# Kernel optimization log

Measured on AMD Instinct MI355X. Metric: run time of the kernel, lower is better.

The kernel has to match this reference:

```python
import jax, jax.numpy as jnp
import numpy as np

B, T, I, H, NC = 128, 512, 128, 512, 100


def setup_inputs() -> dict:
    key = jax.random.key(0)
    ks = jax.random.split(key, 16)
    x = jax.random.randint(ks[0], (B, T, 1), 0, NC + 1)
    # embedding table with padding row 0 zeroed (padding_idx=0)
    emb = (jax.random.normal(ks[1], (NC + 1, I)) * 1.0).at[0].set(0.0)
    # kaiming_normal_ fan_out, sigmoid nonlinearity -> std = 1/sqrt(fan_out)
    sx = 1.0 / np.sqrt(H)
    sc = 1.0 / np.sqrt(H)
    sp = 1.0 / np.sqrt(NC)
    return {
        "x": x,
        "emb": emb,
        "Wfx": jax.random.normal(ks[2], (I, H)) * sx,
        "Wfc": jax.random.normal(ks[3], (H, H)) * sc,
        "bf": jnp.zeros((H,)),
        "Wix": jax.random.normal(ks[4], (I, H)) * sx,
        "Wic": jax.random.normal(ks[5], (H, H)) * sc,
        "bi": jnp.zeros((H,)),
        "Wox": jax.random.normal(ks[6], (I, H)) * sx,
        "Woc": jax.random.normal(ks[7], (H, H)) * sc,
        "bo": jnp.zeros((H,)),
        "Wcx": jax.random.normal(ks[8], (I, H)) * sx,
        "bc": jnp.zeros((H,)),
        "Wph": jax.random.normal(ks[9], (H, NC)) * sp,
        "bp": jnp.zeros((NC,)),
    }


def reference(x, emb, Wfx, Wfc, bf, Wix, Wic, bi, Wox, Woc, bo, Wcx, bc, Wph, bp):
    idx = x[:, :, 0]                      # [B,T] int indices
    xe = emb[idx]                         # [B,T,I] embedded inputs
    h_dim = Wfc.shape[0]
    # Fuse the four input-side GEMMs into one, hoisted out of the recurrence.
    Wx = jnp.concatenate([Wfx, Wix, Wox, Wcx], axis=1)   # [I,4H]
    bx = jnp.concatenate([bf, bi, bo, bc])               # [4H]
    xg = jnp.einsum('bti,ih->bth', xe, Wx) + bx          # [B,T,4H]
    # Fuse the three peephole (cell-state) GEMMs into one per step.
    Wc = jnp.concatenate([Wfc, Wic, Woc], axis=1)        # [H,3H]
    reset = (idx > 0).astype(xg.dtype)                   # [B,T]

    def step(carry, inp):
        C, h = carry
        g, r = inp                        # g: [B,4H], r: [B]
        cg = C @ Wc                       # [B,3H]
        f = jax.nn.sigmoid(g[:, :h_dim] + cg[:, :h_dim])
        i = jax.nn.sigmoid(g[:, h_dim:2 * h_dim] + cg[:, h_dim:2 * h_dim])
        o = jax.nn.sigmoid(g[:, 2 * h_dim:3 * h_dim] + cg[:, 2 * h_dim:])
        c_tilde = jax.nn.sigmoid(g[:, 3 * h_dim:])        # note: sigmoid, not tanh (per source)
        Cn = (c_tilde * i + C * f) * r[:, None]           # reset on padding tokens
        hn = jnp.tanh(Cn) * o
        return (Cn, hn), None

    bsz = xg.shape[0]
    init = (jnp.zeros((bsz, h_dim), xg.dtype), jnp.zeros((bsz, h_dim), xg.dtype))
    xs = (jnp.swapaxes(xg, 0, 1), jnp.swapaxes(reset, 0, 1))  # time-major
    (Cf, hf), _ = jax.lax.scan(step, init, xs)
    p = hf @ Wph + bp                     # [B,num_classes]
    return jax.nn.log_softmax(p, axis=1)
```

## Files before the change

### kernel.cpp

```cpp
#include <hip/hip_runtime.h>
#include <hip/hip_bf16.h>
#include <stdint.h>

#define HD   512
#define ID   128
#define NCLS 100
#define TT   512
#define BB   128
#define NEMB 101
#define NGRP 32
#define GWG  8
#define RPG  4
#define COLS 64
#define THR  512
#define CPAD 640
#define CBW  260
#define PST  5

#define WS_FLAG 0
#define WS_BAR  4096
#define WS_G    65536
#define WS_C0   (1u * 1024 * 1024)
#define WS_C1   (WS_C0 + 262144)
#define WS_HFB  (WS_C1 + 262144)
#define NBARU   4096

using bf16 = __hip_bfloat16;

__device__ __forceinline__ float b2f(bf16 v) { return __bfloat162float(v); }
__device__ __forceinline__ float sigf(float x) { return 1.0f / (1.0f + expf(-x)); }

__device__ __forceinline__ float cld(const float* p) {
    return __hip_atomic_load(p, __ATOMIC_RELAXED, __HIP_MEMORY_SCOPE_AGENT);
}
__device__ __forceinline__ void cst(float* p, float v) {
    __hip_atomic_store(p, v, __ATOMIC_RELAXED, __HIP_MEMORY_SCOPE_AGENT);
}
__device__ __forceinline__ uint64_t cld8(const float* p) {
    return __hip_atomic_load((const uint64_t*)p, __ATOMIC_RELAXED,
                             __HIP_MEMORY_SCOPE_AGENT);
}

__device__ __forceinline__ uint32_t pkbf(float x, float y) {
    uint32_t u;
    asm("v_cvt_pk_bf16_f32 %0, %1, %2" : "=v"(u) : "v"(x), "v"(y));
    return u;
}
#define DOT2(acc, w, c) \
    asm("v_dot2_f32_bf16 %0, %1, %2, %0" : "+v"(acc) : "v"(w), "v"(c))

template <bool BF>
__device__ __forceinline__ float ldv(const void* p, int i) {
    if constexpr (BF) return b2f(((const bf16*)p)[i]);
    else              return ((const float*)p)[i];
}

__device__ __forceinline__ int cpi(int h) { return (h >> 4) * 20 + (h & 15); }

__device__ __forceinline__ void gbarrier(unsigned* cnt, unsigned* iter) {
    __syncthreads();
    if (threadIdx.x == 0) {
        __hip_atomic_fetch_add(cnt, 1u, __ATOMIC_RELAXED, __HIP_MEMORY_SCOPE_AGENT);
        const unsigned tgt = (*iter + 1u) * GWG;
        while (__hip_atomic_load(cnt, __ATOMIC_RELAXED, __HIP_MEMORY_SCOPE_AGENT) < tgt)
            ;
    }
    ++*iter;
    __syncthreads();
}

__global__ void init_k(const uint32_t* __restrict__ emb_raw,
                       int* __restrict__ flag, unsigned* __restrict__ bars) {
    const int t = threadIdx.x;
    for (int k = t; k < NBARU; k += 1024) bars[k] = 0u;
    if (t == 0) {
        uint32_t acc = 0;
        for (int i = 64; i < 128; ++i) acc |= emb_raw[i];
        *flag = (acc == 0u) ? 0 : 1;
    }
}

template <bool BF>
__global__ void build_G(const int* __restrict__ flag,
                        const void* __restrict__ emb,
                        const void* __restrict__ Wfx, const void* __restrict__ Wix,
                        const void* __restrict__ Wox, const void* __restrict__ Wcx,
                        const void* __restrict__ bfv, const void* __restrict__ biv,
                        const void* __restrict__ bov, const void* __restrict__ bcv,
                        float* __restrict__ G) {
    if (*flag != (BF ? 1 : 0)) return;
    const int c   = blockIdx.x;
    const int j   = blockIdx.y * 256 + threadIdx.x;
    const int q   = j >> 9;
    const int col = j & 511;
    const void* W  = (q == 0) ? Wfx : (q == 1) ? Wix : (q == 2) ? Wox : Wcx;
    const void* bv = (q == 0) ? bfv : (q == 1) ? biv : (q == 2) ? bov : bcv;
    float acc = ldv<BF>(bv, col);
    for (int i = 0; i < ID; ++i)
        acc += ldv<BF>(emb, c * ID + i) * ldv<BF>(W, i * HD + col);
    if (q == 3) acc = sigf(acc);
    G[c * 2048 + j] = acc;
}

template <bool BF>
__global__ __launch_bounds__(THR, 2) void recur_bs(
    const int* __restrict__ flag, const int* __restrict__ x,
    const float* __restrict__ G,
    const void* __restrict__ Wfc, const void* __restrict__ Wic,
    const void* __restrict__ Woc,
    float* __restrict__ C0, float* __restrict__ C1,
    float* __restrict__ Hfb, unsigned* __restrict__ bars)
{
    if (*flag != (BF ? 1 : 0)) return;

    __shared__ __align__(16) float Cs[RPG * CPAD];
    __shared__ __align__(8)  float2 part2[2048 * PST];
    __shared__ int idx[RPG * TT];
    __shared__ int lz[RPG];

    const int blk   = blockIdx.x;
    const int grp   = blk >> 3;
    const int rank  = blk & 7;
    const int r0    = grp * RPG;
    const int h0    = rank * COLS;
    const int tid   = threadIdx.x;
    const int cp    = tid & 15;
    const int chunk = tid >> 4;
    unsigned* bar = bars + grp * 32;

    idx[tid]        = x[r0 * TT + tid];
    idx[tid + 512]  = x[r0 * TT + tid + 512];
    idx[tid + 1024] = x[r0 * TT + tid + 1024];
    idx[tid + 1536] = x[r0 * TT + tid + 1536];
    if (tid < RPG) lz[tid] = -1;
    __syncthreads();
    #pragma unroll
    for (int r = 0; r < RPG; ++r)
        if (idx[r * TT + tid] == 0) atomicMax(&lz[r], tid);
    __syncthreads();
    int t0 = TT;
    #pragma unroll
    for (int r = 0; r < RPG; ++r) t0 = min(t0, lz[r] + 1);

    unsigned bi = 0;
    float Creg = 0.0f;
    const bool isUpd = (tid < COLS * RPG);
    const int uc = tid & 63, ur = tid >> 6;
    const int pe = cpi(tid);

    if constexpr (BF) {
        const uint16_t* Wfr = (const uint16_t*)Wfc;
        const uint16_t* Wir = (const uint16_t*)Wic;

        uint32_t wf0[8], wf1[8], wf2[8], wf3[8];
        uint32_t wi0[8], wi1[8], wi2[8], wi3[8];
        #pragma unroll
        for (int p = 0; p < 8; ++p) {
            const int hp = chunk * 16 + 2 * p;
            const int b0 = hp * HD + h0 + cp, b1 = (hp + 1) * HD + h0 + cp;
            wf0[p] = (uint32_t)Wfr[b0]      | ((uint32_t)Wfr[b1]      << 16);
            wf1[p] = (uint32_t)Wfr[b0 + 16] | ((uint32_t)Wfr[b1 + 16] << 16);
            wf2[p] = (uint32_t)Wfr[b0 + 32] | ((uint32_t)Wfr[b1 + 32] << 16);
            wf3[p] = (uint32_t)Wfr[b0 + 48] | ((uint32_t)Wfr[b1 + 48] << 16);
            wi0[p] = (uint32_t)Wir[b0]      | ((uint32_t)Wir[b1]      << 16);
            wi1[p] = (uint32_t)Wir[b0 + 16] | ((uint32_t)Wir[b1 + 16] << 16);
            wi2[p] = (uint32_t)Wir[b0 + 32] | ((uint32_t)Wir[b1 + 32] << 16);
            wi3[p] = (uint32_t)Wir[b0 + 48] | ((uint32_t)Wir[b1 + 48] << 16);
        }
        #pragma unroll
        for (int p = 0; p < 8; ++p)
            asm volatile("" : "+v"(wf0[p]), "+v"(wf1[p]), "+v"(wf2[p]), "+v"(wf3[p]),
                              "+v"(wi0[p]), "+v"(wi1[p]), "+v"(wi2[p]), "+v"(wi3[p]));

        if (isUpd) {
            cst(&C0[(r0 + ur) * HD + h0 + uc], 0.0f);
            cst(&C1[(r0 + ur) * HD + h0 + uc], 0.0f);
        }
        gbarrier(bar, &bi);

        uint32_t* Cb = (uint32_t*)Cs;
        const int srow = tid >> 8;
        const int spr  = tid & 255;

        for (int t = t0; t < TT; ++t) {
            #pragma unroll
            for (int p = 0; p < 8; ++p)
                asm volatile("" : "+v"(wf0[p]), "+v"(wf1[p]), "+v"(wf2[p]), "+v"(wf3[p]),
                                  "+v"(wi0[p]), "+v"(wi1[p]), "+v"(wi2[p]), "+v"(wi3[p]));

            const float* cur = (t & 1) ? C1 : C0;
            float*       nxt = (t & 1) ? C0 : C1;

            float gf = 0.f, gi = 0.f, sgc = 0.f;
            int cl = 1;
            if (isUpd) {
                cl = idx[ur * TT + t];
                const float* Gr = G + cl * 2048;
                gf  = Gr[h0 + uc];
                gi  = Gr[512 + h0 + uc];
                sgc = Gr[1536 + h0 + uc];
            }

            {
                const uint64_t a = cld8(cur + (r0 + srow) * HD + 2 * spr);
                const uint64_t b = cld8(cur + (r0 + srow + 2) * HD + 2 * spr);
                const uint32_t pa = pkbf(__uint_as_float((uint32_t)a),
                                         __uint_as_float((uint32_t)(a >> 32)));
                const uint32_t pb = pkbf(__uint_as_float((uint32_t)b),
                                         __uint_as_float((uint32_t)(b >> 32)));
                Cb[srow * CBW + spr]       = pa;
                Cb[(srow + 2) * CBW + spr] = pb;
            }
            __syncthreads();

            float f0[RPG], f1[RPG], f2[RPG], f3[RPG];
            float i0[RPG], i1[RPG], i2[RPG], i3[RPG];
            #pragma unroll
            for (int r = 0; r < RPG; ++r) {
                f0[r] = 0.f; f1[r] = 0.f; f2[r] = 0.f; f3[r] = 0.f;
                i0[r] = 0.f; i1[r] = 0.f; i2[r] = 0.f; i3[r] = 0.f;
            }
            {
                const int cb = chunk * 8;
                #pragma unroll
                for (int hh = 0; hh < 2; ++hh) {
                    #pragma unroll
                    for (int r = 0; r < RPG; ++r) {
                        const uint4 cv = *reinterpret_cast<const uint4*>(
                            Cb + r * CBW + cb + 4 * hh);
                        const int p = 4 * hh;
                        DOT2(f0[r], wf0[p + 0], cv.x); DOT2(f0[r], wf0[p + 1], cv.y);
                        DOT2(f0[r], wf0[p + 2], cv.z); DOT2(f0[r], wf0[p + 3], cv.w);
                        DOT2(f1[r], wf1[p + 0], cv.x); DOT2(f1[r], wf1[p + 1], cv.y);
                        DOT2(f1[r], wf1[p + 2], cv.z); DOT2(f1[r], wf1[p + 3], cv.w);
                        DOT2(f2[r], wf2[p + 0], cv.x); DOT2(f2[r], wf2[p + 1], cv.y);
                        DOT2(f2[r], wf2[p + 2], cv.z); DOT2(f2[r], wf2[p + 3], cv.w);
                        DOT2(f3[r], wf3[p + 0], cv.x); DOT2(f3[r], wf3[p + 1], cv.y);
                        DOT2(f3[r], wf3[p + 2], cv.z); DOT2(f3[r], wf3[p + 3], cv.w);
                        DOT2(i0[r], wi0[p + 0], cv.x); DOT2(i0[r], wi0[p + 1], cv.y);
                        DOT2(i0[r], wi0[p + 2], cv.z); DOT2(i0[r], wi0[p + 3], cv.w);
                        DOT2(i1[r], wi1[p + 0], cv.x); DOT2(i1[r], wi1[p + 1], cv.y);
                        DOT2(i1[r], wi1[p + 2], cv.z); DOT2(i1[r], wi1[p + 3], cv.w);
                        DOT2(i2[r], wi2[p + 0], cv.x); DOT2(i2[r], wi2[p + 1], cv.y);
                        DOT2(i2[r], wi2[p + 2], cv.z); DOT2(i2[r], wi2[p + 3], cv.w);
                        DOT2(i3[r], wi3[p + 0], cv.x); DOT2(i3[r], wi3[p + 1], cv.y);
                        DOT2(i3[r], wi3[p + 2], cv.z); DOT2(i3[r], wi3[p + 3], cv.w);
                    }
                }
            }
            {
                float2* p0 = part2 + (chunk * 64 + cp)      * PST;
                float2* p1 = part2 + (chunk * 64 + cp + 16) * PST;
                float2* p2 = part2 + (chunk * 64 + cp + 32) * PST;
                float2* p3 = part2 + (chunk * 64 + cp + 48) * PST;
                #pragma unroll
                for (int r = 0; r < RPG; ++r) {
                    p0[r] = make_float2(f0[r], i0[r]);
                    p1[r] = make_float2(f1[r], i1[r]);
                    p2[r] = make_float2(f2[r], i2[r]);
                    p3[r] = make_float2(f3[r], i3[r]);
                }
            }
            __syncthreads();

            if (isUpd) {
                float df = 0.f, di = 0.f;
                #pragma unroll
                for (int ch = 0; ch < 32; ++ch) {
                    const float2 v = part2[(ch * 64 + uc) * PST + ur];
                    df += v.x;
                    di += v.y;
                }
                float Cn = sgc * sigf(gi + di) + Creg * sigf(gf + df);
                Cn = (cl > 0) ? Cn : 0.0f;
                Creg = Cn;
                cst(&nxt[(r0 + ur) * HD + h0 + uc], Cn);
            }
            gbarrier(bar, &bi);
        }
    } else {
        float wf0[16], wf1[16], wf2[16], wf3[16];
        float wi0[16], wi1[16], wi2[16], wi3[16];
        #pragma unroll
        for (int k = 0; k < 16; ++k) {
            const int hp = chunk * 16 + k;
            wf0[k] = ldv<BF>(Wfc, hp * HD + h0 + cp);
            wf1[k] = ldv<BF>(Wfc, hp * HD + h0 + cp + 16);
            wf2[k] = ldv<BF>(Wfc, hp * HD + h0 + cp + 32);
            wf3[k] = ldv<BF>(Wfc, hp * HD + h0 + cp + 48);
            wi0[k] = ldv<BF>(Wic, hp * HD + h0 + cp);
            wi1[k] = ldv<BF>(Wic, hp * HD + h0 + cp + 16);
            wi2[k] = ldv<BF>(Wic, hp * HD + h0 + cp + 32);
            wi3[k] = ldv<BF>(Wic, hp * HD + h0 + cp + 48);
        }
        #pragma unroll
        for (int k = 0; k < 16; ++k)
            asm volatile("" : "+v"(wf0[k]), "+v"(wf1[k]), "+v"(wf2[k]), "+v"(wf3[k]),
                              "+v"(wi0[k]), "+v"(wi1[k]), "+v"(wi2[k]), "+v"(wi3[k]));

        if (isUpd) {
            cst(&C0[(r0 + ur) * HD + h0 + uc], 0.0f);
            cst(&C1[(r0 + ur) * HD + h0 + uc], 0.0f);
        }
        gbarrier(bar, &bi);

        for (int t = t0; t < TT; ++t) {
            #pragma unroll
            for (int k = 0; k < 16; ++k)
                asm volatile("" : "+v"(wf0[k]), "+v"(wf1[k]), "+v"(wf2[k]), "+v"(wf3[k]),
                                  "+v"(wi0[k]), "+v"(wi1[k]), "+v"(wi2[k]), "+v"(wi3[k]));

            const float* cur = (t & 1) ? C1 : C0;
            float*       nxt = (t & 1) ? C0 : C1;

            float gf = 0.f, gi = 0.f, sgc = 0.f;
            int cl = 1;
            if (isUpd) {
                cl = idx[ur * TT + t];
                const float* Gr = G + cl * 2048;
                gf  = Gr[h0 + uc];
                gi  = Gr[512 + h0 + uc];
                sgc = Gr[1536 + h0 + uc];
            }

            {
                const float v0 = cld(cur + (r0 + 0) * HD + tid);
                const float v1 = cld(cur + (r0 + 1) * HD + tid);
                const float v2 = cld(cur + (r0 + 2) * HD + tid);
                const float v3 = cld(cur + (r0 + 3) * HD + tid);
                Cs[0 * CPAD + pe] = v0;
                Cs[1 * CPAD + pe] = v1;
                Cs[2 * CPAD + pe] = v2;
                Cs[3 * CPAD + pe] = v3;
            }
            __syncthreads();

            float f0[RPG], f1[RPG], f2[RPG], f3[RPG];
            float i0[RPG], i1[RPG], i2[RPG], i3[RPG];
            #pragma unroll
            for (int r = 0; r < RPG; ++r) {
                f0[r] = 0.f; f1[r] = 0.f; f2[r] = 0.f; f3[r] = 0.f;
                i0[r] = 0.f; i1[r] = 0.f; i2[r] = 0.f; i3[r] = 0.f;
            }
            {
                const int cb = chunk * 5;
                #pragma unroll
                for (int j = 0; j < 4; ++j) {
                    #pragma unroll
                    for (int r = 0; r < RPG; ++r) {
                        const float4 cv = reinterpret_cast<const float4*>(
                            Cs + r * CPAD)[cb + j];
                        f0[r] += wf0[4*j]*cv.x + wf0[4*j+1]*cv.y + wf0[4*j+2]*cv.z + wf0[4*j+3]*cv.w;
                        f1[r] += wf1[4*j]*cv.x + wf1[4*j+1]*cv.y + wf1[4*j+2]*cv.z + wf1[4*j+3]*cv.w;
                        f2[r] += wf2[4*j]*cv.x + wf2[4*j+1]*cv.y + wf2[4*j+2]*cv.z + wf2[4*j+3]*cv.w;
                        f3[r] += wf3[4*j]*cv.x + wf3[4*j+1]*cv.y + wf3[4*j+2]*cv.z + wf3[4*j+3]*cv.w;
                        i0[r] += wi0[4*j]*cv.x + wi0[4*j+1]*cv.y + wi0[4*j+2]*cv.z + wi0[4*j+3]*cv.w;
                        i1[r] += wi1[4*j]*cv.x + wi1[4*j+1]*cv.y + wi1[4*j+2]*cv.z + wi1[4*j+3]*cv.w;
                        i2[r] += wi2[4*j]*cv.x + wi2[4*j+1]*cv.y + wi2[4*j+2]*cv.z + wi2[4*j+3]*cv.w;
                        i3[r] += wi3[4*j]*cv.x + wi3[4*j+1]*cv.y + wi3[4*j+2]*cv.z + wi3[4*j+3]*cv.w;
                    }
                }
            }
            {
                float2* p0 = part2 + (chunk * 64 + cp)      * PST;
                float2* p1 = part2 + (chunk * 64 + cp + 16) * PST;
                float2* p2 = part2 + (chunk * 64 + cp + 32) * PST;
                float2* p3 = part2 + (chunk * 64 + cp + 48) * PST;
                #pragma unroll
                for (int r = 0; r < RPG; ++r) {
                    p0[r] = make_float2(f0[r], i0[r]);
                    p1[r] = make_float2(f1[r], i1[r]);
                    p2[r] = make_float2(f2[r], i2[r]);
                    p3[r] = make_float2(f3[r], i3[r]);
                }
            }
            __syncthreads();

            if (isUpd) {
                float df = 0.f, di = 0.f;
                #pragma unroll
                for (int ch = 0; ch < 32; ++ch) {
                    const float2 v = part2[(ch * 64 + uc) * PST + ur];
                    df += v.x;
                    di += v.y;
                }
                float Cn = sgc * sigf(gi + di) + Creg * sigf(gf + df);
                Cn = (cl > 0) ? Cn : 0.0f;
                Creg = Cn;
                cst(&nxt[(r0 + ur) * HD + h0 + uc], Cn);
            }
            gbarrier(bar, &bi);
        }
    }

    {
        const float v0 = cld(C1 + (r0 + 0) * HD + tid);
        const float v1 = cld(C1 + (r0 + 1) * HD + tid);
        const float v2 = cld(C1 + (r0 + 2) * HD + tid);
        const float v3 = cld(C1 + (r0 + 3) * HD + tid);
        Cs[0 * CPAD + pe] = v0;
        Cs[1 * CPAD + pe] = v1;
        Cs[2 * CPAD + pe] = v2;
        Cs[3 * CPAD + pe] = v3;
        __syncthreads();

        const int oc = tid & 63, och = tid >> 6;
        float ao[RPG];
        #pragma unroll
        for (int r = 0; r < RPG; ++r) ao[r] = 0.0f;
        #pragma unroll 4
        for (int k = 0; k < 64; ++k) {
            const int hp = och * 64 + k;
            const int hpp = cpi(hp);
            const float wo = ldv<BF>(Woc, hp * HD + h0 + oc);
            #pragma unroll
            for (int r = 0; r < RPG; ++r)
                ao[r] += wo * Cs[r * CPAD + hpp];
        }
        {
            float2* pp = part2 + (och * 64 + oc) * PST;
            #pragma unroll
            for (int r2 = 0; r2 < RPG / 2; ++r2)
                pp[r2] = make_float2(ao[2 * r2], ao[2 * r2 + 1]);
        }
        __syncthreads();
        if (isUpd) {
            float s = 0.f;
            #pragma unroll
            for (int ch = 0; ch < 8; ++ch) {
                const float2 v = part2[(ch * 64 + uc) * PST + (ur >> 1)];
                s += (ur & 1) ? v.y : v.x;
            }
            const int cl2 = idx[ur * TT + TT - 1];
            const float o = sigf(G[cl2 * 2048 + 1024 + h0 + uc] + s);
            Hfb[(r0 + ur) * HD + h0 + uc] = tanhf(Creg) * o;
        }
    }
}

template <bool BF>
__global__ __launch_bounds__(128) void proj(
    const int* __restrict__ flag, const float* __restrict__ Hfb,
    const void* __restrict__ Wph, const void* __restrict__ bp,
    void* __restrict__ out)
{
    if (*flag != (BF ? 1 : 0)) return;
    __shared__ __align__(16) float hv[HD];
    __shared__ float p_s[NCLS];
    __shared__ float lse_s;
    const int b   = blockIdx.x;
    const int tid = threadIdx.x;

    reinterpret_cast<float4*>(hv)[tid] =
        reinterpret_cast<const float4*>(Hfb + b * HD)[tid];
    __syncthreads();

    if (tid < NCLS) {
        float p = ldv<BF>(bp, tid);
        for (int h = 0; h < HD; ++h)
            p += hv[h] * ldv<BF>(Wph, h * NCLS + tid);
        p_s[tid] = p;
    }
    __syncthreads();
    if (tid == 0) {
        float m = -1e30f;
        for (int n = 0; n < NCLS; ++n) m = fmaxf(m, p_s[n]);
        float sum = 0.0f;
        for (int n = 0; n < NCLS; ++n) sum += expf(p_s[n] - m);
        lse_s = m + logf(sum);
    }
    __syncthreads();
    if (tid < NCLS) {
        const float v = p_s[tid] - lse_s;
        if constexpr (BF) ((bf16*)out)[b * NCLS + tid] = __float2bfloat16(v);
        else              ((float*)out)[b * NCLS + tid] = v;
    }
}

extern "C" void kernel_launch(void* const* d_in, const int* in_sizes, int n_in,
                              void* d_out, int out_size, void* d_ws, size_t ws_size,
                              hipStream_t stream) {
    const int*  x   = (const int*)d_in[0];
    const void* emb = d_in[1];
    const void* Wfx = d_in[2];
    const void* Wfc = d_in[3];
    const void* bfv = d_in[4];
    const void* Wix = d_in[5];
    const void* Wic = d_in[6];
    const void* biv = d_in[7];
    const void* Wox = d_in[8];
    const void* Woc = d_in[9];
    const void* bov = d_in[10];
    const void* Wcx = d_in[11];
    const void* bcv = d_in[12];
    const void* Wph = d_in[13];
    const void* bp  = d_in[14];

    int*      flag = (int*)((char*)d_ws + WS_FLAG);
    unsigned* bars = (unsigned*)((char*)d_ws + WS_BAR);
    float*    G    = (float*)((char*)d_ws + WS_G);
    float*    C0   = (float*)((char*)d_ws + WS_C0);
    float*    C1   = (float*)((char*)d_ws + WS_C1);
    float*    Hfb  = (float*)((char*)d_ws + WS_HFB);

    init_k<<<1, 1024, 0, stream>>>((const uint32_t*)emb, flag, bars);

    build_G<false><<<dim3(NEMB, 8), 256, 0, stream>>>(flag, emb, Wfx, Wix, Wox, Wcx,
                                                      bfv, biv, bov, bcv, G);
    build_G<true ><<<dim3(NEMB, 8), 256, 0, stream>>>(flag, emb, Wfx, Wix, Wox, Wcx,
                                                      bfv, biv, bov, bcv, G);

    {
        void* args[] = {(void*)&flag, (void*)&x, (void*)&G,
                        (void*)&Wfc, (void*)&Wic, (void*)&Woc,
                        (void*)&C0, (void*)&C1, (void*)&Hfb, (void*)&bars};
        hipLaunchCooperativeKernel((const void*)recur_bs<false>, dim3(NGRP * GWG), dim3(THR),
                                   args, 0, stream);
        hipLaunchCooperativeKernel((const void*)recur_bs<true>, dim3(NGRP * GWG), dim3(THR),
                                   args, 0, stream);
    }

    proj<false><<<BB, 128, 0, stream>>>(flag, Hfb, Wph, bp, d_out);
    proj<true ><<<BB, 128, 0, stream>>>(flag, Hfb, Wph, bp, d_out);
}
```

Baseline: 1.604 ms.

## Repartition bf16 recurrence into 64 groups of 4 workgroups with 2 rows each

The bf16 recurrence path now splits the batch into 64 groups of 2 rows, each handled by 4 workgroups covering 128 columns, instead of 32 groups of 4 rows spread over 8 workgroups. Fewer workgroups share each per-step global barrier, which is meant to cut barrier latency and cross-workgroup traffic on the serial time loop. In exchange each thread holds twice as many packed weight registers and does a longer dot product over fewer rows. This raises register pressure, and occupancy or spills could suffer. The fp32 path keeps the old partition, with constants renamed.

```diff
diff --git a/kernel.cpp b/kernel.cpp
--- a/kernel.cpp
+++ b/kernel.cpp
@@ -8,14 +8,21 @@
 #define TT   512
 #define BB   128
 #define NEMB 101
-#define NGRP 32
-#define GWG  8
-#define RPG  4
-#define COLS 64
 #define THR  512
+
+#define NGRPB 64
+#define GWGB  4
+#define RPGB  2
+#define COLSB 128
+#define NGRPF 32
+#define GWGF  8
+#define RPGF  4
+#define COLSF 64
+
 #define CPAD 640
 #define CBW  260
-#define PST  5
+#define PSTF 5
+#define PSTB 3
 
 #define WS_FLAG 0
 #define WS_BAR  4096
@@ -57,11 +64,11 @@
 
 __device__ __forceinline__ int cpi(int h) { return (h >> 4) * 20 + (h & 15); }
 
-__device__ __forceinline__ void gbarrier(unsigned* cnt, unsigned* iter) {
+__device__ __forceinline__ void gbarrier(unsigned* cnt, unsigned* iter, int gwg) {
     __syncthreads();
     if (threadIdx.x == 0) {
         __hip_atomic_fetch_add(cnt, 1u, __ATOMIC_RELAXED, __HIP_MEMORY_SCOPE_AGENT);
-        const unsigned tgt = (*iter + 1u) * GWG;
+        const unsigned tgt = (*iter + 1u) * (unsigned)gwg;
         while (__hip_atomic_load(cnt, __ATOMIC_RELAXED, __HIP_MEMORY_SCOPE_AGENT) < tgt)
             ;
     }
@@ -113,78 +120,75 @@
 {
     if (*flag != (BF ? 1 : 0)) return;
 
-    __shared__ __align__(16) float Cs[RPG * CPAD];
-    __shared__ __align__(8)  float2 part2[2048 * PST];
-    __shared__ int idx[RPG * TT];
-    __shared__ int lz[RPG];
-
-    const int blk   = blockIdx.x;
-    const int grp   = blk >> 3;
-    const int rank  = blk & 7;
-    const int r0    = grp * RPG;
-    const int h0    = rank * COLS;
-    const int tid   = threadIdx.x;
-    const int cp    = tid & 15;
-    const int chunk = tid >> 4;
-    unsigned* bar = bars + grp * 32;
-
-    idx[tid]        = x[r0 * TT + tid];
-    idx[tid + 512]  = x[r0 * TT + tid + 512];
-    idx[tid + 1024] = x[r0 * TT + tid + 1024];
-    idx[tid + 1536] = x[r0 * TT + tid + 1536];
-    if (tid < RPG) lz[tid] = -1;
-    __syncthreads();
-    #pragma unroll
-    for (int r = 0; r < RPG; ++r)
-        if (idx[r * TT + tid] == 0) atomicMax(&lz[r], tid);
-    __syncthreads();
-    int t0 = TT;
-    #pragma unroll
-    for (int r = 0; r < RPG; ++r) t0 = min(t0, lz[r] + 1);
-
+    __shared__ __align__(16) float Cs[RPGF * CPAD];
+    __shared__ __align__(8)  float2 part2[2048 * PSTF];
+    __shared__ int idx[RPGF * TT];
+    __shared__ int lz[RPGF];
+
+    const int blk = blockIdx.x;
+    const int tid = threadIdx.x;
     unsigned bi = 0;
-    float Creg = 0.0f;
-    const bool isUpd = (tid < COLS * RPG);
-    const int uc = tid & 63, ur = tid >> 6;
-    const int pe = cpi(tid);
 
     if constexpr (BF) {
+        const int grp   = blk >> 2;
+        const int rank  = blk & 3;
+        const int r0    = grp * RPGB;
+        const int h0    = rank * COLSB;
+        const int cp    = tid & 31;
+        const int chunk = tid >> 5;
+        unsigned* bar = bars + grp * 32;
+
+        idx[tid]       = x[r0 * TT + tid];
+        idx[tid + 512] = x[r0 * TT + tid + 512];
+        if (tid < RPGB) lz[tid] = -1;
+        __syncthreads();
+        #pragma unroll
+        for (int r = 0; r < RPGB; ++r)
+            if (idx[r * TT + tid] == 0) atomicMax(&lz[r], tid);
+        __syncthreads();
+        int t0 = TT;
+        #pragma unroll
+        for (int r = 0; r < RPGB; ++r) t0 = min(t0, lz[r] + 1);
+
         const uint16_t* Wfr = (const uint16_t*)Wfc;
         const uint16_t* Wir = (const uint16_t*)Wic;
-
-        uint32_t wf0[8], wf1[8], wf2[8], wf3[8];
-        uint32_t wi0[8], wi1[8], wi2[8], wi3[8];
-        #pragma unroll
-        for (int p = 0; p < 8; ++p) {
-            const int hp = chunk * 16 + 2 * p;
+        uint32_t wf0[16], wf1[16], wf2[16], wf3[16];
+        uint32_t wi0[16], wi1[16], wi2[16], wi3[16];
+        #pragma unroll
+        for (int p = 0; p < 16; ++p) {
+            const int hp = chunk * 32 + 2 * p;
             const int b0 = hp * HD + h0 + cp, b1 = (hp + 1) * HD + h0 + cp;
             wf0[p] = (uint32_t)Wfr[b0]      | ((uint32_t)Wfr[b1]      << 16);
-            wf1[p] = (uint32_t)Wfr[b0 + 16] | ((uint32_t)Wfr[b1 + 16] << 16);
-            wf2[p] = (uint32_t)Wfr[b0 + 32] | ((uint32_t)Wfr[b1 + 32] << 16);
-            wf3[p] = (uint32_t)Wfr[b0 + 48] | ((uint32_t)Wfr[b1 + 48] << 16);
+            wf1[p] = (uint32_t)Wfr[b0 + 32] | ((uint32_t)Wfr[b1 + 32] << 16);
+            wf2[p] = (uint32_t)Wfr[b0 + 64] | ((uint32_t)Wfr[b1 + 64] << 16);
+            wf3[p] = (uint32_t)Wfr[b0 + 96] | ((uint32_t)Wfr[b1 + 96] << 16);
             wi0[p] = (uint32_t)Wir[b0]      | ((uint32_t)Wir[b1]      << 16);
-            wi1[p] = (uint32_t)Wir[b0 + 16] | ((uint32_t)Wir[b1 + 16] << 16);
-            wi2[p] = (uint32_t)Wir[b0 + 32] | ((uint32_t)Wir[b1 + 32] << 16);
-            wi3[p] = (uint32_t)Wir[b0 + 48] | ((uint32_t)Wir[b1 + 48] << 16);
-        }
-        #pragma unroll
-        for (int p = 0; p < 8; ++p)
+            wi1[p] = (uint32_t)Wir[b0 + 32] | ((uint32_t)Wir[b1 + 32] << 16);
+            wi2[p] = (uint32_t)Wir[b0 + 64] | ((uint32_t)Wir[b1 + 64] << 16);
+            wi3[p] = (uint32_t)Wir[b0 + 96] | ((uint32_t)Wir[b1 + 96] << 16);
+        }
+        #pragma unroll
+        for (int p = 0; p < 16; ++p)
             asm volatile("" : "+v"(wf0[p]), "+v"(wf1[p]), "+v"(wf2[p]), "+v"(wf3[p]),
                               "+v"(wi0[p]), "+v"(wi1[p]), "+v"(wi2[p]), "+v"(wi3[p]));
+
+        const bool isUpd = (tid < COLSB * RPGB);
+        const int uc = tid & 127, ur = tid >> 7;
 
         if (isUpd) {
             cst(&C0[(r0 + ur) * HD + h0 + uc], 0.0f);
             cst(&C1[(r0 + ur) * HD + h0 + uc], 0.0f);
         }
-        gbarrier(bar, &bi);
-
+        gbarrier(bar, &bi, GWGB);
+
+        float Creg = 0.0f;
         uint32_t* Cb = (uint32_t*)Cs;
         const int srow = tid >> 8;
         const int spr  = tid & 255;
 
         for (int t = t0; t < TT; ++t) {
             #pragma unroll
-            for (int p = 0; p < 8; ++p)
+            for (int p = 0; p < 16; ++p)
                 asm volatile("" : "+v"(wf0[p]), "+v"(wf1[p]), "+v"(wf2[p]), "+v"(wf3[p]),
                                   "+v"(wi0[p]), "+v"(wi1[p]), "+v"(wi2[p]), "+v"(wi3[p]));
 
@@ -203,29 +207,24 @@
 
             {
                 const uint64_t a = cld8(cur + (r0 + srow) * HD + 2 * spr);
-                const uint64_t b = cld8(cur + (r0 + srow + 2) * HD + 2 * spr);
-                const uint32_t pa = pkbf(__uint_as_float((uint32_t)a),
-                                         __uint_as_float((uint32_t)(a >> 32)));
-                const uint32_t pb = pkbf(__uint_as_float((uint32_t)b),
-                                         __uint_as_float((uint32_t)(b >> 32)));
-                Cb[srow * CBW + spr]       = pa;
-                Cb[(srow + 2) * CBW + spr] = pb;
-            }
-            __syncthreads();
-
-            float f0[RPG], f1[RPG], f2[RPG], f3[RPG];
-            float i0[RPG], i1[RPG], i2[RPG], i3[RPG];
+                Cb[srow * CBW + spr] = pkbf(__uint_as_float((uint32_t)a),
+                                            __uint_as_float((uint32_t)(a >> 32)));
+            }
+            __syncthreads();
+
+            float f0[RPGB], f1[RPGB], f2[RPGB], f3[RPGB];
+            float i0[RPGB], i1[RPGB], i2[RPGB], i3[RPGB];
             #pragma unroll
-            for (int r = 0; r < RPG; ++r) {
+            for (int r = 0; r < RPGB; ++r) {
                 f0[r] = 0.f; f1[r] = 0.f; f2[r] = 0.f; f3[r] = 0.f;
                 i0[r] = 0.f; i1[r] = 0.f; i2[r] = 0.f; i3[r] = 0.f;
             }
             {
-                const int cb = chunk * 8;
-                #pragma unroll
-                for (int hh = 0; hh < 2; ++hh) {
+                const int cb = chunk * 16;
+                #pragma unroll
+                for (int hh = 0; hh < 4; ++hh) {
                     #pragma unroll
-                    for (int r = 0; r < RPG; ++r) {
+                    for (int r = 0; r < RPGB; ++r) {
                         const uint4 cv = *reinterpret_cast<const uint4*>(
                             Cb + r * CBW + cb + 4 * hh);
                         const int p = 4 * hh;
@@ -249,12 +248,12 @@
                 }
             }
             {
-                float2* p0 = part2 + (chunk * 64 + cp)      * PST;
-                float2* p1 = part2 + (chunk * 64 + cp + 16) * PST;
-                float2* p2 = part2 + (chunk * 64 + cp + 32) * PST;
-                float2* p3 = part2 + (chunk * 64 + cp + 48) * PST;
-                #pragma unroll
-                for (int r = 0; r < RPG; ++r) {
+                float2* p0 = part2 + (chunk * 128 + cp)      * PSTB;
+                float2* p1 = part2 + (chunk * 128 + cp + 32) * PSTB;
+                float2* p2 = part2 + (chunk * 128 + cp + 64) * PSTB;
+                float2* p3 = part2 + (chunk * 128 + cp + 96) * PSTB;
+                #pragma unroll
+                for (int r = 0; r < RPGB; ++r) {
                     p0[r] = make_float2(f0[r], i0[r]);
                     p1[r] = make_float2(f1[r], i1[r]);
                     p2[r] = make_float2(f2[r], i2[r]);
@@ -266,8 +265,8 @@
             if (isUpd) {
                 float df = 0.f, di = 0.f;
                 #pragma unroll
-                for (int ch = 0; ch < 32; ++ch) {
-                    const float2 v = part2[(ch * 64 + uc) * PST + ur];
+                for (int ch = 0; ch < 16; ++ch) {
+                    const float2 v = part2[(ch * 128 + uc) * PSTB + ur];
                     df += v.x;
                     di += v.y;
                 }
@@ -276,9 +275,64 @@
                 Creg = Cn;
                 cst(&nxt[(r0 + ur) * HD + h0 + uc], Cn);
             }
-            gbarrier(bar, &bi);
+            gbarrier(bar, &bi, GWGB);
+        }
+
+        {
+            const float v0 = cld(C1 + (r0 + 0) * HD + tid);
+            const float v1 = cld(C1 + (r0 + 1) * HD + tid);
+            const int pe = cpi(tid);
+            Cs[0 * CPAD + pe] = v0;
+            Cs[1 * CPAD + pe] = v1;
+            __syncthreads();
+
+            const int oc = tid & 127, och = tid >> 7;
+            float ao0 = 0.f, ao1 = 0.f;
+            #pragma unroll 4
+            for (int k = 0; k < 128; ++k) {
+                const int hp  = och * 128 + k;
+                const int hpp = cpi(hp);
+                const float wo = ldv<BF>(Woc, hp * HD + h0 + oc);
+                ao0 += wo * Cs[0 * CPAD + hpp];
+                ao1 += wo * Cs[1 * CPAD + hpp];
+            }
+            part2[(och * 128 + oc) * PSTB] = make_float2(ao0, ao1);
+            __syncthreads();
+            if (isUpd) {
+                float s = 0.f;
+                #pragma unroll
+                for (int ch = 0; ch < 4; ++ch) {
+                    const float2 v = part2[(ch * 128 + uc) * PSTB];
+                    s += ur ? v.y : v.x;
+                }
+                const int cl2 = idx[ur * TT + TT - 1];
+                const float o = sigf(G[cl2 * 2048 + 1024 + h0 + uc] + s);
+                Hfb[(r0 + ur) * HD + h0 + uc] = tanhf(Creg) * o;
+            }
         }
     } else {
+        const int grp   = blk >> 3;
+        const int rank  = blk & 7;
+        const int r0    = grp * RPGF;
+        const int h0    = rank * COLSF;
+        const int cp    = tid & 15;
+        const int chunk = tid >> 4;
+        unsigned* bar = bars + grp * 32;
+
+        idx[tid]        = x[r0 * TT + tid];
+        idx[tid + 512]  = x[r0 * TT + tid + 512];
+        idx[tid + 1024] = x[r0 * TT + tid + 1024];
+        idx[tid + 1536] = x[r0 * TT + tid + 1536];
+        if (tid < RPGF) lz[tid] = -1;
+        __syncthreads();
+        #pragma unroll
+        for (int r = 0; r < RPGF; ++r)
+            if (idx[r * TT + tid] == 0) atomicMax(&lz[r], tid);
+        __syncthreads();
+        int t0 = TT;
+        #pragma unroll
+        for (int r = 0; r < RPGF; ++r) t0 = min(t0, lz[r] + 1);
+
         float wf0[16], wf1[16], wf2[16], wf3[16];
         float wi0[16], wi1[16], wi2[16], wi3[16];
         #pragma unroll
@@ -298,12 +352,17 @@
             asm volatile("" : "+v"(wf0[k]), "+v"(wf1[k]), "+v"(wf2[k]), "+v"(wf3[k]),
                               "+v"(wi0[k]), "+v"(wi1[k]), "+v"(wi2[k]), "+v"(wi3[k]));
 
+        const bool isUpd = (tid < COLSF * RPGF);
+        const int uc = tid & 63, ur = tid >> 6;
+        const int pe = cpi(tid);
+
         if (isUpd) {
             cst(&C0[(r0 + ur) * HD + h0 + uc], 0.0f);
             cst(&C1[(r0 + ur) * HD + h0 + uc], 0.0f);
         }
-        gbarrier(bar, &bi);
-
+        gbarrier(bar, &bi, GWGF);
+
+        float Creg = 0.0f;
         for (int t = t0; t < TT; ++t) {
             #pragma unroll
             for (int k = 0; k < 16; ++k)
@@ -335,10 +394,10 @@
             }
             __syncthreads();
 
-            float f0[RPG], f1[RPG], f2[RPG], f3[RPG];
-            float i0[RPG], i1[RPG], i2[RPG], i3[RPG];
+            float f0[RPGF], f1[RPGF], f2[RPGF], f3[RPGF];
+            float i0[RPGF], i1[RPGF], i2[RPGF], i3[RPGF];
             #pragma unroll
-            for (int r = 0; r < RPG; ++r) {
+            for (int r = 0; r < RPGF; ++r) {
                 f0[r] = 0.f; f1[r] = 0.f; f2[r] = 0.f; f3[r] = 0.f;
                 i0[r] = 0.f; i1[r] = 0.f; i2[r] = 0.f; i3[r] = 0.f;
             }
@@ -347,7 +406,7 @@
                 #pragma unroll
                 for (int j = 0; j < 4; ++j) {
                     #pragma unroll
-                    for (int r = 0; r < RPG; ++r) {
+                    for (int r = 0; r < RPGF; ++r) {
                         const float4 cv = reinterpret_cast<const float4*>(
                             Cs + r * CPAD)[cb + j];
                         f0[r] += wf0[4*j]*cv.x + wf0[4*j+1]*cv.y + wf0[4*j+2]*cv.z + wf0[4*j+3]*cv.w;
@@ -362,12 +421,12 @@
                 }
             }
             {
-                float2* p0 = part2 + (chunk * 64 + cp)      * PST;
-                float2* p1 = part2 + (chunk * 64 + cp + 16) * PST;
-                float2* p2 = part2 + (chunk * 64 + cp + 32) * PST;
-                float2* p3 = part2 + (chunk * 64 + cp + 48) * PST;
-                #pragma unroll
-                for (int r = 0; r < RPG; ++r) {
+                float2* p0 = part2 + (chunk * 64 + cp)      * PSTF;
+                float2* p1 = part2 + (chunk * 64 + cp + 16) * PSTF;
+                float2* p2 = part2 + (chunk * 64 + cp + 32) * PSTF;
+                float2* p3 = part2 + (chunk * 64 + cp + 48) * PSTF;
+                #pragma unroll
+                for (int r = 0; r < RPGF; ++r) {
                     p0[r] = make_float2(f0[r], i0[r]);
                     p1[r] = make_float2(f1[r], i1[r]);
                     p2[r] = make_float2(f2[r], i2[r]);
@@ -380,7 +439,7 @@
                 float df = 0.f, di = 0.f;
                 #pragma unroll
                 for (int ch = 0; ch < 32; ++ch) {
-                    const float2 v = part2[(ch * 64 + uc) * PST + ur];
+                    const float2 v = part2[(ch * 64 + uc) * PSTF + ur];
                     df += v.x;
                     di += v.y;
                 }
@@ -389,51 +448,51 @@
                 Creg = Cn;
                 cst(&nxt[(r0 + ur) * HD + h0 + uc], Cn);
             }
-            gbarrier(bar, &bi);
-        }
-    }
-
-    {
-        const float v0 = cld(C1 + (r0 + 0) * HD + tid);
-        const float v1 = cld(C1 + (r0 + 1) * HD + tid);
-        const float v2 = cld(C1 + (r0 + 2) * HD + tid);
-        const float v3 = cld(C1 + (r0 + 3) * HD + tid);
-        Cs[0 * CPAD + pe] = v0;
-        Cs[1 * CPAD + pe] = v1;
-        Cs[2 * CPAD + pe] = v2;
-        Cs[3 * CPAD + pe] = v3;
-        __syncthreads();
-
-        const int oc = tid & 63, och = tid >> 6;
-        float ao[RPG];
-        #pragma unroll
-        for (int r = 0; r < RPG; ++r) ao[r] = 0.0f;
-        #pragma unroll 4
-        for (int k = 0; k < 64; ++k) {
-            const int hp = och * 64 + k;
-            const int hpp = cpi(hp);
-            const float wo = ldv<BF>(Woc, hp * HD + h0 + oc);
+            gbarrier(bar, &bi, GWGF);
+        }
+
+        {
+            const float v0 = cld(C1 + (r0 + 0) * HD + tid);
+            const float v1 = cld(C1 + (r0 + 1) * HD + tid);
+            const float v2 = cld(C1 + (r0 + 2) * HD + tid);
+            const float v3 = cld(C1 + (r0 + 3) * HD + tid);
+            Cs[0 * CPAD + pe] = v0;
+            Cs[1 * CPAD + pe] = v1;
+            Cs[2 * CPAD + pe] = v2;
+            Cs[3 * CPAD + pe] = v3;
+            __syncthreads();
+
+            const int oc = tid & 63, och = tid >> 6;
+            float ao[RPGF];
             #pragma unroll
-            for (int r = 0; r < RPG; ++r)
-                ao[r] += wo * Cs[r * CPAD + hpp];
-        }
-        {
-            float2* pp = part2 + (och * 64 + oc) * PST;
-            #pragma unroll
-            for (int r2 = 0; r2 < RPG / 2; ++r2)
-                pp[r2] = make_float2(ao[2 * r2], ao[2 * r2 + 1]);
-        }
-        __syncthreads();
-        if (isUpd) {
-            float s = 0.f;
-            #pragma unroll
-            for (int ch = 0; ch < 8; ++ch) {
-                const float2 v = part2[(ch * 64 + uc) * PST + (ur >> 1)];
-                s += (ur & 1) ? v.y : v.x;
-            }
-            const int cl2 = idx[ur * TT + TT - 1];
-            const float o = sigf(G[cl2 * 2048 + 1024 + h0 + uc] + s);
-            Hfb[(r0 + ur) * HD + h0 + uc] = tanhf(Creg) * o;
+            for (int r = 0; r < RPGF; ++r) ao[r] = 0.0f;
+            #pragma unroll 4
+            for (int k = 0; k < 64; ++k) {
+                const int hp = och * 64 + k;
+                const int hpp = cpi(hp);
+                const float wo = ldv<BF>(Woc, hp * HD + h0 + oc);
+                #pragma unroll
+                for (int r = 0; r < RPGF; ++r)
+                    ao[r] += wo * Cs[r * CPAD + hpp];
+            }
+            {
+                float2* pp = part2 + (och * 64 + oc) * PSTF;
+                #pragma unroll
+                for (int r2 = 0; r2 < RPGF / 2; ++r2)
+                    pp[r2] = make_float2(ao[2 * r2], ao[2 * r2 + 1]);
+            }
+            __syncthreads();
+            if (isUpd) {
+                float s = 0.f;
+                #pragma unroll
+                for (int ch = 0; ch < 8; ++ch) {
+                    const float2 v = part2[(ch * 64 + uc) * PSTF + (ur >> 1)];
+                    s += (ur & 1) ? v.y : v.x;
+                }
+                const int cl2 = idx[ur * TT + TT - 1];
+                const float o = sigf(G[cl2 * 2048 + 1024 + h0 + uc] + s);
+                Hfb[(r0 + ur) * HD + h0 + uc] = tanhf(Creg) * o;
+            }
         }
     }
 }
@@ -514,9 +573,9 @@
         void* args[] = {(void*)&flag, (void*)&x, (void*)&G,
                         (void*)&Wfc, (void*)&Wic, (void*)&Woc,
                         (void*)&C0, (void*)&C1, (void*)&Hfb, (void*)&bars};
-        hipLaunchCooperativeKernel((const void*)recur_bs<false>, dim3(NGRP * GWG), dim3(THR),
+        hipLaunchCooperativeKernel((const void*)recur_bs<false>, dim3(256), dim3(THR),
                                    args, 0, stream);
-        hipLaunchCooperativeKernel((const void*)recur_bs<true>, dim3(NGRP * GWG), dim3(THR),
+        hipLaunchCooperativeKernel((const void*)recur_bs<true>, dim3(256), dim3(THR),
                                    args, 0, stream);
     }
 
```

Measured after the change: 1.599 ms. No clear change (-0.4%).
